# Kernel tuning notes

Measured on AMD Instinct MI355X. Metric: run time of the kernel, lower is better.

## Reference

```python
import jax, jax.numpy as jnp
import numpy as np

B, S, H = 512, 200, 256

def setup_inputs() -> dict:
    key = jax.random.key(0)
    ks = jax.random.split(key, 7)
    scale = 1.0 / np.sqrt(H)
    return {
        "all_memory": jax.random.normal(ks[0], (B, S, H), dtype=jnp.float32),
        "last_memory": jax.random.normal(ks[1], (B, H), dtype=jnp.float32),
        "U": jax.random.normal(ks[2], (H, H), dtype=jnp.float32) * scale,   # U_meta weight
        "W": jax.random.normal(ks[3], (H, H), dtype=jnp.float32) * scale,   # W_meta weight
        "V": jax.random.normal(ks[4], (H, 1), dtype=jnp.float32) * scale,   # V_meta weight (stored as [H,1])
        "MetaW": jax.random.normal(ks[5], (4, H), dtype=jnp.float32) * scale,  # Meta weight
        "Metab": jax.random.normal(ks[6], (4,), dtype=jnp.float32) * scale,    # Meta bias ('multiple' mode)
    }

def reference(all_memory, last_memory, U, W, V, MetaW, Metab):
    # U_meta(all_memory): [B,S,H]; W_meta(last_memory): [B,H] broadcast over S
    a = jnp.einsum('bsh,kh->bsk', all_memory, U)
    l = jnp.einsum('bh,kh->bk', last_memory, W)
    # additive attention score: V_meta(tanh(a + l)) -> [B,S]
    scores = jnp.einsum('bsh,h->bs', jnp.tanh(a + l[:, None, :]), V[:, 0])
    alpha = jax.nn.softmax(scores, axis=1)  # softmax over seq dim
    pooled = jnp.einsum('bs,bsh->bh', alpha, all_memory)  # weighted sum of values
    return pooled @ MetaW.T + Metab  # [B, 4]
```

## Files before the change

### kernel.cpp

```cpp
#include <hip/hip_runtime.h>
#include <hip/hip_bf16.h>
#include <math.h>

#define NB 512
#define NS 200
#define NH 256
#define TILE_S 32
#define LDSPAD 8
#define LDW (NH + LDSPAD)
#define WS_STRIDE 258
#define NPART (NB * 2)

#define OFF_PART 0
#define OFF_L    (NPART * WS_STRIDE)
#define OFF_UB   (OFF_L + NB * NH)
#define WS_FLOATS_PRE  (OFF_UB + (NH * NH) / 2)

typedef __bf16 bf16x8 __attribute__((ext_vector_type(8)));
typedef float  f32x4  __attribute__((ext_vector_type(4)));

__device__ __forceinline__ float tanh_fast(float x) {
  float xc = fminf(fmaxf(x, -10.f), 10.f);
  float e  = __expf(2.f * xc);
  return (e - 1.f) / (e + 1.f);
}

__global__ __launch_bounds__(256)
void precompute(const float* __restrict__ lastm, const float* __restrict__ W,
                const float* __restrict__ U,
                float* __restrict__ l_ws, __bf16* __restrict__ Uswz)
{
  const int t = threadIdx.x;
  if (blockIdx.x < NB) {
    const int b = blockIdx.x;
    __shared__ float lm_sm[NH];
    lm_sm[t] = lastm[(size_t)b * NH + t];
    __syncthreads();
    const float4* wrow = (const float4*)(W + (size_t)t * NH);
    const float4* lrow = (const float4*)lm_sm;
    float a0 = 0.f, a1 = 0.f, a2 = 0.f, a3 = 0.f;
#pragma unroll 8
    for (int i = 0; i < NH / 4; ++i) {
      float4 w4 = wrow[i];
      float4 m4 = lrow[i];
      a0 = fmaf(w4.x, m4.x, a0);
      a1 = fmaf(w4.y, m4.y, a1);
      a2 = fmaf(w4.z, m4.z, a2);
      a3 = fmaf(w4.w, m4.w, a3);
    }
    l_ws[(size_t)b * NH + t] = (a0 + a1) + (a2 + a3);
  } else {
    const int id    = (blockIdx.x - NB) * 256 + t;
    const int n_blk = id >> 9;
    const int kk    = (id >> 6) & 7;
    const int lane  = id & 63;
    const int row   = n_blk * 16 + (lane & 15);
    const int col   = kk * 32 + (lane >> 4) * 8;
    const float4* s = (const float4*)(U + (size_t)row * NH + col);
    const float4 a = s[0], c = s[1];
    bf16x8 pk;
    pk[0] = (__bf16)a.x; pk[1] = (__bf16)a.y;
    pk[2] = (__bf16)a.z; pk[3] = (__bf16)a.w;
    pk[4] = (__bf16)c.x; pk[5] = (__bf16)c.y;
    pk[6] = (__bf16)c.z; pk[7] = (__bf16)c.w;
    *(bf16x8*)(Uswz + (size_t)id * 8) = pk;
  }
}

template<bool PRE>
__global__ __launch_bounds__(256, 2)
void fused_meta_attn_part(const float* __restrict__ mem,
                          const float* __restrict__ lastm,
                          const float* __restrict__ U,
                          const float* __restrict__ W,
                          const float* __restrict__ V,
                          const float* __restrict__ l_ws,
                          const __bf16* __restrict__ Uswz,
                          float* __restrict__ part)
{
  const int b    = blockIdx.x >> 1;
  const int half = blockIdx.x & 1;
  const int s_begin = half ? 96 : 0;
  const int s_end   = half ? NS : 96;
  const int ntiles  = half ? 4 : 3;

  const int t    = threadIdx.x;
  const int wave = t >> 6;
  const int lane = t & 63;
  const int m16  = lane & 15;
  const int quad = lane >> 4;

  __shared__ __align__(16) __bf16 mem_sm[TILE_S][LDW];
  __shared__ float swave_sm[4][TILE_S];
  __shared__ float scores_sm[TILE_S];
  __shared__ float l_sm[NH];
  __shared__ float lm_sm[NH];

  if (!PRE) {
    lm_sm[t] = lastm[(size_t)b * NH + t];
    __syncthreads();
    const float4* wrow = (const float4*)(W + (size_t)t * NH);
    const float4* lrow = (const float4*)lm_sm;
    float a0 = 0.f, a1 = 0.f, a2 = 0.f, a3 = 0.f;
#pragma unroll 8
    for (int i = 0; i < NH / 4; ++i) {
      float4 w4 = wrow[i];
      float4 m4 = lrow[i];
      a0 = fmaf(w4.x, m4.x, a0);
      a1 = fmaf(w4.y, m4.y, a1);
      a2 = fmaf(w4.z, m4.z, a2);
      a3 = fmaf(w4.w, m4.w, a3);
    }
    l_sm[t] = (a0 + a1) + (a2 + a3);
    __syncthreads();
  }

  float l_reg[4], v_reg[4];
#pragma unroll
  for (int nf = 0; nf < 4; ++nf) {
    const int n = wave * 64 + nf * 16 + m16;
    l_reg[nf] = PRE ? l_ws[(size_t)b * NH + n] : l_sm[n];
    v_reg[nf] = V[n];
  }

  bf16x8 u_frag[4][8];
  if (PRE) {
    const __bf16* uw = Uswz + ((size_t)(wave * 4 * 8 * 64) + lane) * 8;
#pragma unroll
    for (int nf = 0; nf < 4; ++nf)
#pragma unroll
      for (int kk = 0; kk < 8; ++kk)
        u_frag[nf][kk] = *(const bf16x8*)(uw + (size_t)((nf * 8 + kk) << 9));
  } else {
#pragma unroll
    for (int nf = 0; nf < 4; ++nf) {
      const int n = wave * 64 + nf * 16 + m16;
      const float* urow = U + (size_t)n * NH;
#pragma unroll
      for (int kk = 0; kk < 8; ++kk) {
        const float4 lo = *(const float4*)(urow + kk * 32 + quad * 8);
        const float4 hi = *(const float4*)(urow + kk * 32 + quad * 8 + 4);
        bf16x8 f;
        f[0] = (__bf16)lo.x; f[1] = (__bf16)lo.y;
        f[2] = (__bf16)lo.z; f[3] = (__bf16)lo.w;
        f[4] = (__bf16)hi.x; f[5] = (__bf16)hi.y;
        f[6] = (__bf16)hi.z; f[7] = (__bf16)hi.w;
        u_frag[nf][kk] = f;
      }
    }
  }

  float m_run  = -INFINITY;
  float Z      = 0.f;
  float pooled = 0.f;

  for (int tile = 0; tile < ntiles; ++tile) {
    const int s0   = s_begin + tile * TILE_S;
    const int rows = min(TILE_S, s_end - s0);

    const float4* src4 = (const float4*)(mem + ((size_t)b * NS + s0) * NH);
#pragma unroll
    for (int i = 0; i < 4; ++i) {
      const int f2  = i * 256 + t;
      const int row = f2 >> 5;
      const int c8  = (f2 & 31) * 8;
      bf16x8 pk;
      if (row < rows) {
        const float4 a = src4[f2 * 2];
        const float4 c = src4[f2 * 2 + 1];
        pk[0] = (__bf16)a.x; pk[1] = (__bf16)a.y;
        pk[2] = (__bf16)a.z; pk[3] = (__bf16)a.w;
        pk[4] = (__bf16)c.x; pk[5] = (__bf16)c.y;
        pk[6] = (__bf16)c.z; pk[7] = (__bf16)c.w;
      } else {
        pk = (bf16x8)(__bf16)0.f;
      }
      *(bf16x8*)&mem_sm[row][c8] = pk;
    }
    __syncthreads();

    f32x4 acc[2][4];
    const f32x4 fzero = {0.f, 0.f, 0.f, 0.f};
#pragma unroll
    for (int mt = 0; mt < 2; ++mt)
#pragma unroll
      for (int nf = 0; nf < 4; ++nf)
        acc[mt][nf] = fzero;

#pragma unroll
    for (int kk = 0; kk < 8; ++kk) {
      const int c = kk * 32 + quad * 8;
      bf16x8 a0 = *(const bf16x8*)&mem_sm[m16][c];
      bf16x8 a1 = *(const bf16x8*)&mem_sm[16 + m16][c];
#pragma unroll
      for (int nf = 0; nf < 4; ++nf) {
        acc[0][nf] = __builtin_amdgcn_mfma_f32_16x16x32_bf16(a0, u_frag[nf][kk], acc[0][nf], 0, 0, 0);
        acc[1][nf] = __builtin_amdgcn_mfma_f32_16x16x32_bf16(a1, u_frag[nf][kk], acc[1][nf], 0, 0, 0);
      }
    }

    float p[2][4];
#pragma unroll
    for (int mt = 0; mt < 2; ++mt) {
#pragma unroll
      for (int reg = 0; reg < 4; ++reg) {
        float s = 0.f;
#pragma unroll
        for (int nf = 0; nf < 4; ++nf)
          s = fmaf(tanh_fast(acc[mt][nf][reg] + l_reg[nf]), v_reg[nf], s);
        p[mt][reg] = s;
      }
    }
#pragma unroll
    for (int off = 1; off < 16; off <<= 1) {
#pragma unroll
      for (int mt = 0; mt < 2; ++mt)
#pragma unroll
        for (int reg = 0; reg < 4; ++reg)
          p[mt][reg] += __shfl_xor(p[mt][reg], off);
    }
    if (m16 == 0) {
#pragma unroll
      for (int mt = 0; mt < 2; ++mt)
#pragma unroll
        for (int reg = 0; reg < 4; ++reg)
          swave_sm[wave][mt * 16 + quad * 4 + reg] = p[mt][reg];
    }
    __syncthreads();

    if (t < TILE_S)
      scores_sm[t] = swave_sm[0][t] + swave_sm[1][t] + swave_sm[2][t] + swave_sm[3][t];
    __syncthreads();

    float m_tile = -INFINITY;
    for (int r = 0; r < rows; ++r) m_tile = fmaxf(m_tile, scores_sm[r]);
    const float m_new = fmaxf(m_run, m_tile);
    const float fac   = __expf(m_run - m_new);
    float z_t = 0.f, pool_t = 0.f;
    for (int r = 0; r < rows; ++r) {
      const float e = __expf(scores_sm[r] - m_new);
      z_t += e;
      pool_t = fmaf(e, (float)mem_sm[r][t], pool_t);
    }
    Z      = Z * fac + z_t;
    pooled = pooled * fac + pool_t;
    m_run  = m_new;
    __syncthreads();
  }

  float* base = part + (size_t)blockIdx.x * WS_STRIDE;
  if (t == 0) { base[0] = m_run; base[1] = Z; }
  base[2 + t] = pooled;
}

__global__ __launch_bounds__(256)
void merge_project(const float* __restrict__ part,
                   const float* __restrict__ MetaW,
                   const float* __restrict__ Metab,
                   float* __restrict__ out)
{
  const int b    = blockIdx.x;
  const int t    = threadIdx.x;
  const int wave = t >> 6;
  const int lane = t & 63;

  __shared__ float pooled_sm[NH];

  const float* b0 = part + (size_t)(b * 2)     * WS_STRIDE;
  const float* b1 = part + (size_t)(b * 2 + 1) * WS_STRIDE;
  const float m0 = b0[0], Z0 = b0[1];
  const float m1 = b1[0], Z1 = b1[1];
  const float mm = fmaxf(m0, m1);
  const float w0 = __expf(m0 - mm);
  const float w1 = __expf(m1 - mm);
  const float Zi = 1.f / (Z0 * w0 + Z1 * w1);

  pooled_sm[t] = (b0[2 + t] * w0 + b1[2 + t] * w1) * Zi;
  __syncthreads();

  float s = 0.f;
#pragma unroll
  for (int i = 0; i < 4; ++i) {
    const int h = i * 64 + lane;
    s = fmaf(pooled_sm[h], MetaW[(size_t)wave * NH + h], s);
  }
#pragma unroll
  for (int off = 32; off > 0; off >>= 1)
    s += __shfl_down(s, off);
  if (lane == 0)
    out[b * 4 + wave] = s + Metab[wave];
}

extern "C" void kernel_launch(void* const* d_in, const int* in_sizes, int n_in,
                              void* d_out, int out_size, void* d_ws, size_t ws_size,
                              hipStream_t stream) {
  const float* mem   = (const float*)d_in[0];
  const float* lastm = (const float*)d_in[1];
  const float* U     = (const float*)d_in[2];
  const float* W     = (const float*)d_in[3];
  const float* V     = (const float*)d_in[4];
  const float* MetaW = (const float*)d_in[5];
  const float* Metab = (const float*)d_in[6];
  float* out = (float*)d_out;
  float* ws  = (float*)d_ws;

  float* part = ws + OFF_PART;

  if (ws_size >= (size_t)WS_FLOATS_PRE * sizeof(float)) {
    float*  l_ws = ws + OFF_L;
    __bf16* Uswz = (__bf16*)(ws + OFF_UB);
    hipLaunchKernelGGL(precompute, dim3(NB + 32), dim3(256), 0, stream,
                       lastm, W, U, l_ws, Uswz);
    hipLaunchKernelGGL(fused_meta_attn_part<true>, dim3(NPART), dim3(256), 0, stream,
                       mem, lastm, U, W, V, l_ws, Uswz, part);
  } else {
    hipLaunchKernelGGL(fused_meta_attn_part<false>, dim3(NPART), dim3(256), 0, stream,
                       mem, lastm, U, W, V, (const float*)nullptr, (const __bf16*)nullptr, part);
  }
  hipLaunchKernelGGL(merge_project, dim3(NB), dim3(256), 0, stream,
                     part, MetaW, Metab, out);
}
```

Measured before the change: 211.7 us.

## Split fused attention into per-tile scores kernel and separate softmax-pool kernel

Replaces the per-half-sequence fused online-softmax kernel with a scores kernel launched per 32-row tile (more blocks) that writes raw scores to workspace. A new 512-thread kernel then does a full softmax per batch and re-reads the fp32 memory to pool and project. This removes the serial per-tile softmax and pooling loop and increases parallelism, at the cost of a second full read of the memory tensor and a scores round trip through global memory. The U fragment setup is now repeated per tile block.

```diff
diff --git a/kernel.cpp b/kernel.cpp
--- a/kernel.cpp
+++ b/kernel.cpp
@@ -6,15 +6,15 @@
 #define NS 200
 #define NH 256
 #define TILE_S 32
+#define NTILE 7
 #define LDSPAD 8
 #define LDW (NH + LDSPAD)
-#define WS_STRIDE 258
-#define NPART (NB * 2)
-
-#define OFF_PART 0
-#define OFF_L    (NPART * WS_STRIDE)
-#define OFF_UB   (OFF_L + NB * NH)
-#define WS_FLOATS_PRE  (OFF_UB + (NH * NH) / 2)
+
+#define OFF_SC 0
+#define OFF_L  (NB * NS)
+#define OFF_UB (OFF_L + NB * NH)
+#define WS_FLOATS_PRE (OFF_UB + (NH * NH) / 2)
+#define WS_FLOATS_MIN (NB * NS)
 
 typedef __bf16 bf16x8 __attribute__((ext_vector_type(8)));
 typedef float  f32x4  __attribute__((ext_vector_type(4)));
@@ -69,20 +69,20 @@
 
 template<bool PRE>
 __global__ __launch_bounds__(256, 2)
-void fused_meta_attn_part(const float* __restrict__ mem,
-                          const float* __restrict__ lastm,
-                          const float* __restrict__ U,
-                          const float* __restrict__ W,
-                          const float* __restrict__ V,
-                          const float* __restrict__ l_ws,
-                          const __bf16* __restrict__ Uswz,
-                          float* __restrict__ part)
+void scores_kernel(const float* __restrict__ mem,
+                   const float* __restrict__ lastm,
+                   const float* __restrict__ U,
+                   const float* __restrict__ W,
+                   const float* __restrict__ V,
+                   const float* __restrict__ l_ws,
+                   const __bf16* __restrict__ Uswz,
+                   float* __restrict__ scores)
 {
-  const int b    = blockIdx.x >> 1;
-  const int half = blockIdx.x & 1;
-  const int s_begin = half ? 96 : 0;
-  const int s_end   = half ? NS : 96;
-  const int ntiles  = half ? 4 : 3;
+  const int blk  = blockIdx.x;
+  const int b    = blk / NTILE;
+  const int tile = blk - b * NTILE;
+  const int s0   = tile * TILE_S;
+  const int rows = min(TILE_S, NS - s0);
 
   const int t    = threadIdx.x;
   const int wave = t >> 6;
@@ -92,7 +92,6 @@
 
   __shared__ __align__(16) __bf16 mem_sm[TILE_S][LDW];
   __shared__ float swave_sm[4][TILE_S];
-  __shared__ float scores_sm[TILE_S];
   __shared__ float l_sm[NH];
   __shared__ float lm_sm[NH];
 
@@ -150,145 +149,160 @@
     }
   }
 
-  float m_run  = -INFINITY;
-  float Z      = 0.f;
-  float pooled = 0.f;
-
-  for (int tile = 0; tile < ntiles; ++tile) {
-    const int s0   = s_begin + tile * TILE_S;
-    const int rows = min(TILE_S, s_end - s0);
-
-    const float4* src4 = (const float4*)(mem + ((size_t)b * NS + s0) * NH);
-#pragma unroll
-    for (int i = 0; i < 4; ++i) {
-      const int f2  = i * 256 + t;
-      const int row = f2 >> 5;
-      const int c8  = (f2 & 31) * 8;
-      bf16x8 pk;
-      if (row < rows) {
-        const float4 a = src4[f2 * 2];
-        const float4 c = src4[f2 * 2 + 1];
-        pk[0] = (__bf16)a.x; pk[1] = (__bf16)a.y;
-        pk[2] = (__bf16)a.z; pk[3] = (__bf16)a.w;
-        pk[4] = (__bf16)c.x; pk[5] = (__bf16)c.y;
-        pk[6] = (__bf16)c.z; pk[7] = (__bf16)c.w;
-      } else {
-        pk = (bf16x8)(__bf16)0.f;
-      }
-      *(bf16x8*)&mem_sm[row][c8] = pk;
-    }
-    __syncthreads();
-
-    f32x4 acc[2][4];
-    const f32x4 fzero = {0.f, 0.f, 0.f, 0.f};
+  const float4* src4 = (const float4*)(mem + ((size_t)b * NS + s0) * NH);
+#pragma unroll
+  for (int i = 0; i < 4; ++i) {
+    const int f2  = i * 256 + t;
+    const int row = f2 >> 5;
+    const int c8  = (f2 & 31) * 8;
+    bf16x8 pk;
+    if (row < rows) {
+      const float4 a = src4[f2 * 2];
+      const float4 c = src4[f2 * 2 + 1];
+      pk[0] = (__bf16)a.x; pk[1] = (__bf16)a.y;
+      pk[2] = (__bf16)a.z; pk[3] = (__bf16)a.w;
+      pk[4] = (__bf16)c.x; pk[5] = (__bf16)c.y;
+      pk[6] = (__bf16)c.z; pk[7] = (__bf16)c.w;
+    } else {
+      pk = (bf16x8)(__bf16)0.f;
+    }
+    *(bf16x8*)&mem_sm[row][c8] = pk;
+  }
+  __syncthreads();
+
+  f32x4 acc[2][4];
+  const f32x4 fzero = {0.f, 0.f, 0.f, 0.f};
+#pragma unroll
+  for (int mt = 0; mt < 2; ++mt)
+#pragma unroll
+    for (int nf = 0; nf < 4; ++nf)
+      acc[mt][nf] = fzero;
+
+#pragma unroll
+  for (int kk = 0; kk < 8; ++kk) {
+    const int c = kk * 32 + quad * 8;
+    bf16x8 a0 = *(const bf16x8*)&mem_sm[m16][c];
+    bf16x8 a1 = *(const bf16x8*)&mem_sm[16 + m16][c];
+#pragma unroll
+    for (int nf = 0; nf < 4; ++nf) {
+      acc[0][nf] = __builtin_amdgcn_mfma_f32_16x16x32_bf16(a0, u_frag[nf][kk], acc[0][nf], 0, 0, 0);
+      acc[1][nf] = __builtin_amdgcn_mfma_f32_16x16x32_bf16(a1, u_frag[nf][kk], acc[1][nf], 0, 0, 0);
+    }
+  }
+
+  float p[2][4];
+#pragma unroll
+  for (int mt = 0; mt < 2; ++mt) {
+#pragma unroll
+    for (int reg = 0; reg < 4; ++reg) {
+      float s = 0.f;
+#pragma unroll
+      for (int nf = 0; nf < 4; ++nf)
+        s = fmaf(tanh_fast(acc[mt][nf][reg] + l_reg[nf]), v_reg[nf], s);
+      p[mt][reg] = s;
+    }
+  }
+#pragma unroll
+  for (int off = 1; off < 16; off <<= 1) {
 #pragma unroll
     for (int mt = 0; mt < 2; ++mt)
 #pragma unroll
-      for (int nf = 0; nf < 4; ++nf)
-        acc[mt][nf] = fzero;
-
-#pragma unroll
-    for (int kk = 0; kk < 8; ++kk) {
-      const int c = kk * 32 + quad * 8;
-      bf16x8 a0 = *(const bf16x8*)&mem_sm[m16][c];
-      bf16x8 a1 = *(const bf16x8*)&mem_sm[16 + m16][c];
-#pragma unroll
-      for (int nf = 0; nf < 4; ++nf) {
-        acc[0][nf] = __builtin_amdgcn_mfma_f32_16x16x32_bf16(a0, u_frag[nf][kk], acc[0][nf], 0, 0, 0);
-        acc[1][nf] = __builtin_amdgcn_mfma_f32_16x16x32_bf16(a1, u_frag[nf][kk], acc[1][nf], 0, 0, 0);
-      }
-    }
-
-    float p[2][4];
-#pragma unroll
-    for (int mt = 0; mt < 2; ++mt) {
-#pragma unroll
-      for (int reg = 0; reg < 4; ++reg) {
-        float s = 0.f;
-#pragma unroll
-        for (int nf = 0; nf < 4; ++nf)
-          s = fmaf(tanh_fast(acc[mt][nf][reg] + l_reg[nf]), v_reg[nf], s);
-        p[mt][reg] = s;
-      }
-    }
-#pragma unroll
-    for (int off = 1; off < 16; off <<= 1) {
-#pragma unroll
-      for (int mt = 0; mt < 2; ++mt)
-#pragma unroll
-        for (int reg = 0; reg < 4; ++reg)
-          p[mt][reg] += __shfl_xor(p[mt][reg], off);
-    }
-    if (m16 == 0) {
-#pragma unroll
-      for (int mt = 0; mt < 2; ++mt)
-#pragma unroll
-        for (int reg = 0; reg < 4; ++reg)
-          swave_sm[wave][mt * 16 + quad * 4 + reg] = p[mt][reg];
-    }
-    __syncthreads();
-
-    if (t < TILE_S)
-      scores_sm[t] = swave_sm[0][t] + swave_sm[1][t] + swave_sm[2][t] + swave_sm[3][t];
-    __syncthreads();
-
-    float m_tile = -INFINITY;
-    for (int r = 0; r < rows; ++r) m_tile = fmaxf(m_tile, scores_sm[r]);
-    const float m_new = fmaxf(m_run, m_tile);
-    const float fac   = __expf(m_run - m_new);
-    float z_t = 0.f, pool_t = 0.f;
-    for (int r = 0; r < rows; ++r) {
-      const float e = __expf(scores_sm[r] - m_new);
-      z_t += e;
-      pool_t = fmaf(e, (float)mem_sm[r][t], pool_t);
-    }
-    Z      = Z * fac + z_t;
-    pooled = pooled * fac + pool_t;
-    m_run  = m_new;
-    __syncthreads();
-  }
-
-  float* base = part + (size_t)blockIdx.x * WS_STRIDE;
-  if (t == 0) { base[0] = m_run; base[1] = Z; }
-  base[2 + t] = pooled;
-}
-
-__global__ __launch_bounds__(256)
-void merge_project(const float* __restrict__ part,
-                   const float* __restrict__ MetaW,
-                   const float* __restrict__ Metab,
-                   float* __restrict__ out)
+      for (int reg = 0; reg < 4; ++reg)
+        p[mt][reg] += __shfl_xor(p[mt][reg], off);
+  }
+  if (m16 == 0) {
+#pragma unroll
+    for (int mt = 0; mt < 2; ++mt)
+#pragma unroll
+      for (int reg = 0; reg < 4; ++reg)
+        swave_sm[wave][mt * 16 + quad * 4 + reg] = p[mt][reg];
+  }
+  __syncthreads();
+
+  if (t < rows)
+    scores[(size_t)b * NS + s0 + t] =
+        swave_sm[0][t] + swave_sm[1][t] + swave_sm[2][t] + swave_sm[3][t];
+}
+
+__global__ __launch_bounds__(512)
+void softmax_pool(const float* __restrict__ scores,
+                  const float* __restrict__ mem,
+                  const float* __restrict__ MetaW,
+                  const float* __restrict__ Metab,
+                  float* __restrict__ out)
 {
   const int b    = blockIdx.x;
   const int t    = threadIdx.x;
   const int wave = t >> 6;
   const int lane = t & 63;
 
+  __shared__ float alpha_sm[NS];
+  __shared__ float red_sm[8];
+  __shared__ __align__(16) float part_sm[8][NH];
   __shared__ float pooled_sm[NH];
 
-  const float* b0 = part + (size_t)(b * 2)     * WS_STRIDE;
-  const float* b1 = part + (size_t)(b * 2 + 1) * WS_STRIDE;
-  const float m0 = b0[0], Z0 = b0[1];
-  const float m1 = b1[0], Z1 = b1[1];
-  const float mm = fmaxf(m0, m1);
-  const float w0 = __expf(m0 - mm);
-  const float w1 = __expf(m1 - mm);
-  const float Zi = 1.f / (Z0 * w0 + Z1 * w1);
-
-  pooled_sm[t] = (b0[2 + t] * w0 + b1[2 + t] * w1) * Zi;
-  __syncthreads();
-
-  float s = 0.f;
-#pragma unroll
-  for (int i = 0; i < 4; ++i) {
-    const int h = i * 64 + lane;
-    s = fmaf(pooled_sm[h], MetaW[(size_t)wave * NH + h], s);
-  }
+  float sv = (t < NS) ? scores[(size_t)b * NS + t] : -INFINITY;
+
+  float wm = sv;
 #pragma unroll
   for (int off = 32; off > 0; off >>= 1)
-    s += __shfl_down(s, off);
-  if (lane == 0)
-    out[b * 4 + wave] = s + Metab[wave];
+    wm = fmaxf(wm, __shfl_xor(wm, off));
+  if (lane == 0) red_sm[wave] = wm;
+  __syncthreads();
+  float m = red_sm[0];
+#pragma unroll
+  for (int w = 1; w < 8; ++w) m = fmaxf(m, red_sm[w]);
+
+  float e = (t < NS) ? __expf(sv - m) : 0.f;
+  float wsum = e;
+#pragma unroll
+  for (int off = 32; off > 0; off >>= 1)
+    wsum += __shfl_xor(wsum, off);
+  __syncthreads();
+  if (lane == 0) red_sm[wave] = wsum;
+  __syncthreads();
+  float Z = 0.f;
+#pragma unroll
+  for (int w = 0; w < 8; ++w) Z += red_sm[w];
+  const float Zi = 1.f / Z;
+
+  if (t < NS) alpha_sm[t] = e * Zi;
+  __syncthreads();
+
+  f32x4 acc4 = {0.f, 0.f, 0.f, 0.f};
+  const f32x4* memb = (const f32x4*)(mem + (size_t)b * NS * NH);
+  for (int r = wave; r < NS; r += 8) {
+    const float a = alpha_sm[r];
+    const f32x4 v4 = memb[(size_t)r * (NH / 4) + lane];
+    acc4[0] = fmaf(a, v4[0], acc4[0]);
+    acc4[1] = fmaf(a, v4[1], acc4[1]);
+    acc4[2] = fmaf(a, v4[2], acc4[2]);
+    acc4[3] = fmaf(a, v4[3], acc4[3]);
+  }
+  *(f32x4*)&part_sm[wave][lane * 4] = acc4;
+  __syncthreads();
+
+  if (t < NH) {
+    float s = 0.f;
+#pragma unroll
+    for (int w = 0; w < 8; ++w) s += part_sm[w][t];
+    pooled_sm[t] = s;
+  }
+  __syncthreads();
+
+  if (wave < 4) {
+    float s = 0.f;
+#pragma unroll
+    for (int i = 0; i < 4; ++i) {
+      const int h = i * 64 + lane;
+      s = fmaf(pooled_sm[h], MetaW[(size_t)wave * NH + h], s);
+    }
+#pragma unroll
+    for (int off = 32; off > 0; off >>= 1)
+      s += __shfl_down(s, off);
+    if (lane == 0)
+      out[b * 4 + wave] = s + Metab[wave];
+  }
 }
 
 extern "C" void kernel_launch(void* const* d_in, const int* in_sizes, int n_in,
@@ -304,19 +318,19 @@
   float* out = (float*)d_out;
   float* ws  = (float*)d_ws;
 
-  float* part = ws + OFF_PART;
+  float* scores = ws + OFF_SC;
 
   if (ws_size >= (size_t)WS_FLOATS_PRE * sizeof(float)) {
     float*  l_ws = ws + OFF_L;
     __bf16* Uswz = (__bf16*)(ws + OFF_UB);
     hipLaunchKernelGGL(precompute, dim3(NB + 32), dim3(256), 0, stream,
                        lastm, W, U, l_ws, Uswz);
-    hipLaunchKernelGGL(fused_meta_attn_part<true>, dim3(NPART), dim3(256), 0, stream,
-                       mem, lastm, U, W, V, l_ws, Uswz, part);
+    hipLaunchKernelGGL(scores_kernel<true>, dim3(NB * NTILE), dim3(256), 0, stream,
+                       mem, lastm, U, W, V, l_ws, Uswz, scores);
   } else {
-    hipLaunchKernelGGL(fused_meta_attn_part<false>, dim3(NPART), dim3(256), 0, stream,
-                       mem, lastm, U, W, V, (const float*)nullptr, (const __bf16*)nullptr, part);
-  }
-  hipLaunchKernelGGL(merge_project, dim3(NB), dim3(256), 0, stream,
-                     part, MetaW, Metab, out);
-}
+    hipLaunchKernelGGL(scores_kernel<false>, dim3(NB * NTILE), dim3(256), 0, stream,
+                       mem, lastm, U, W, V, (const float*)nullptr, (const __bf16*)nullptr, scores);
+  }
+  hipLaunchKernelGGL(softmax_pool, dim3(NB), dim3(512), 0, stream,
+                     scores, mem, MetaW, Metab, out);
+}
```

Result: no change. 213.9 us (+1.0%).
